# Optimization experiments

Hardware: AMD Instinct MI355X
Metric: run time of the kernel (lower is better)

Reference implementation:

```python
import jax, jax.numpy as jnp
import numpy as np

INPUT_SIZE = 512
HIDDEN_SIZE = 1024
BATCH = 32
SEQ = 512


def setup_inputs() -> dict:
    key = jax.random.key(0)
    ks = jax.random.split(key, 13)
    std = 1.0 / np.sqrt(HIDDEN_SIZE)
    u = lambda k, shape: jax.random.uniform(k, shape, jnp.float32, -std, std)
    X = jax.random.normal(ks[0], (BATCH, SEQ, INPUT_SIZE), jnp.float32)
    return {
        "X": X,
        "w_i": u(ks[1], (INPUT_SIZE, HIDDEN_SIZE)), "u_i": u(ks[2], (HIDDEN_SIZE, HIDDEN_SIZE)), "b_i": u(ks[3], (HIDDEN_SIZE,)),
        "w_f": u(ks[4], (INPUT_SIZE, HIDDEN_SIZE)), "u_f": u(ks[5], (HIDDEN_SIZE, HIDDEN_SIZE)), "b_f": u(ks[6], (HIDDEN_SIZE,)),
        "w_c": u(ks[7], (INPUT_SIZE, HIDDEN_SIZE)), "u_c": u(ks[8], (HIDDEN_SIZE, HIDDEN_SIZE)), "b_c": u(ks[9], (HIDDEN_SIZE,)),
        "w_o": u(ks[10], (INPUT_SIZE, HIDDEN_SIZE)), "u_o": u(ks[11], (HIDDEN_SIZE, HIDDEN_SIZE)), "b_o": u(ks[12], (HIDDEN_SIZE,)),
    }


def reference(X, w_i, u_i, b_i, w_f, u_f, b_f, w_c, u_c, b_c, w_o, u_o, b_o):
    bs, seq, _ = X.shape
    H = u_i.shape[0]
    # Precompute input-side projections for all gates in one batched matmul.
    W = jnp.concatenate([w_i, w_f, w_c, w_o], axis=1)        # [I, 4H]
    b = jnp.concatenate([b_i, b_f, b_c, b_o], axis=0)        # [4H]
    Xg = jnp.einsum("bsi,ig->bsg", X, W) + b                 # [B, S, 4H]
    Xg = jnp.transpose(Xg, (1, 0, 2))                         # [S, B, 4H]
    U = jnp.concatenate([u_i, u_f, u_c, u_o], axis=1)         # [H, 4H]

    def step(carry, xg_t):
        h, c = carry
        g = xg_t + h @ U                                       # [B, 4H]
        i_t = jax.nn.sigmoid(g[:, 0:H])
        f_t = jax.nn.sigmoid(g[:, H:2 * H])
        g_t = jnp.tanh(g[:, 2 * H:3 * H])
        o_t = jax.nn.sigmoid(g[:, 3 * H:4 * H])
        c_new = f_t * c + i_t * g_t
        h_new = o_t * jnp.tanh(c_new)
        return (h_new, c_new), h_new

    h0 = jnp.zeros((bs, H), X.dtype)
    c0 = jnp.zeros((bs, H), X.dtype)
    (h_t, c_t), hidden_seq = jax.lax.scan(step, (h0, c0), Xg)  # hidden_seq: [S, B, H]
    hidden_seq = jnp.transpose(hidden_seq, (1, 0, 2))          # [B, S, H]
    return hidden_seq, (h_t, c_t)
```

## Files before the change

kernel.cpp:

```cpp
#include <hip/hip_runtime.h>

typedef unsigned short u16;
typedef unsigned int   u32;

typedef __bf16 bf16x8 __attribute__((ext_vector_type(8)));
typedef float  f32x4  __attribute__((ext_vector_type(4)));
typedef u32    u32x4  __attribute__((ext_vector_type(4)));

#define B_ 32
#define S_ 512
#define I_ 512
#define H_ 1024
#define NB 64
#define UB 16
#define CB 64

#define XBF_U16   (S_ * B_ * I_)
#define HSLOT_B   65536

__device__ __forceinline__ u16 bf16bits(float f) {
    __bf16 b = (__bf16)f;
    return __builtin_bit_cast(u16, b);
}
__device__ __forceinline__ float sigmoid_(float x) { return 1.0f / (1.0f + __expf(-x)); }
__device__ __forceinline__ float tanh_(float x)    { return 2.0f / (1.0f + __expf(-2.0f * x)) - 1.0f; }

__global__ void __launch_bounds__(256)
xcvt(const float* __restrict__ X, u16* __restrict__ xbf)
{
    const int t = blockIdx.x, tid = threadIdx.x;
    #pragma unroll 4
    for (int b = 0; b < B_; ++b) {
        float2 v = *(const float2*)(X + (size_t)b * (S_ * I_) + (size_t)t * I_ + tid * 2);
        u32 pk = (u32)bf16bits(v.x) | ((u32)bf16bits(v.y) << 16);
        *(u32*)(xbf + (size_t)t * (B_ * I_) + b * I_ + tid * 2) = pk;
    }
}

__global__ void __launch_bounds__(512, 2)
lstm_rec(const u16* __restrict__ xbf,
         const float* __restrict__ u_i, const float* __restrict__ b_i,
         const float* __restrict__ u_f, const float* __restrict__ b_f,
         const float* __restrict__ u_c, const float* __restrict__ b_c,
         const float* __restrict__ u_o, const float* __restrict__ b_o,
         const float* __restrict__ w_i, const float* __restrict__ w_f,
         const float* __restrict__ w_c, const float* __restrict__ w_o,
         float* __restrict__ out, u16* __restrict__ hsl, u32* __restrict__ flags)
{
    __shared__ __align__(16) char  hx[32 * 3072];
    __shared__ __align__(16) float gb[4][32][68];

    const int tid  = threadIdx.x;
    const int bid  = blockIdx.x;
    const int wave = tid >> 6;
    const int lane = tid & 63;
    const int quad = lane >> 4;
    const int l16  = lane & 15;
    const int cg   = wave & 1;
    const int kq   = wave >> 1;

    bf16x8 bfr[2][12];
    #pragma unroll
    for (int cs = 0; cs < 2; ++cs) {
        const int gc = bid * CB + cg * 32 + cs * 16 + l16;
        const int ug = gc >> 2, g = gc & 3;
        const float* Up = ((g == 0) ? u_i : (g == 1) ? u_f : (g == 2) ? u_c : u_o) + ug;
        const float* Wp = ((g == 0) ? w_i : (g == 1) ? w_f : (g == 2) ? w_c : w_o) + ug;
        #pragma unroll
        for (int kb = 0; kb < 12; ++kb) {
            const int kbg = kq * 12 + kb;
            #pragma unroll
            for (int j = 0; j < 8; ++j) {
                const int k = kbg * 32 + quad * 8 + j;
                bfr[cs][kb][j] = (k < 1024) ? (__bf16)Up[(size_t)k * H_]
                                            : (__bf16)Wp[(size_t)(k - 1024) * H_];
            }
        }
    }

    const int srow = tid & 31;
    const int sch  = tid >> 5;
    const int skey = (srow & 7) << 4;
    char* sdst = hx + srow * 3072;
    const int akey = (l16 & 7) << 4;

    const int ub2  = tid >> 4;
    const int uq   = tid & 15;
    const int unit = bid * UB + uq;
    const float bia = b_i[unit], bif = b_f[unit], bic = b_c[unit], bio = b_o[unit];
    float cst = 0.0f;

    for (int t = 0; t < S_; ++t) {
        const u32x4* xsrc = (const u32x4*)(xbf + (size_t)t * (B_ * I_) + srow * I_ + sch * 32);
        u32x4 xv0 = xsrc[0], xv1 = xsrc[1], xv2 = xsrc[2], xv3 = xsrc[3];

        if (t) {
            if (wave == 0) {
                const u32* fp = flags + lane * 16;
                u32 v;
                do {
                    asm volatile("global_load_dword %0, %1, off sc0 sc1\n\t"
                                 "s_waitcnt vmcnt(0)"
                                 : "=v"(v) : "v"(fp) : "memory");
                } while ((int)v < t);
            }
            asm volatile("s_barrier" ::: "memory");

            const char* hsrc = (const char*)hsl + (size_t)(t & 1) * HSLOT_B
                               + srow * 2048 + sch * 128;
            u32x4 h0, h1, h2, h3, h4, h5, h6, h7;
            asm volatile(
                "global_load_dwordx4 %0, %8, off sc0 sc1\n\t"
                "global_load_dwordx4 %1, %8, off offset:16 sc0 sc1\n\t"
                "global_load_dwordx4 %2, %8, off offset:32 sc0 sc1\n\t"
                "global_load_dwordx4 %3, %8, off offset:48 sc0 sc1\n\t"
                "global_load_dwordx4 %4, %8, off offset:64 sc0 sc1\n\t"
                "global_load_dwordx4 %5, %8, off offset:80 sc0 sc1\n\t"
                "global_load_dwordx4 %6, %8, off offset:96 sc0 sc1\n\t"
                "global_load_dwordx4 %7, %8, off offset:112 sc0 sc1\n\t"
                "s_waitcnt vmcnt(0)"
                : "=&v"(h0), "=&v"(h1), "=&v"(h2), "=&v"(h3),
                  "=&v"(h4), "=&v"(h5), "=&v"(h6), "=&v"(h7)
                : "v"(hsrc) : "memory");
            *(u32x4*)(sdst + ((sch * 128 +   0) ^ skey)) = h0;
            *(u32x4*)(sdst + ((sch * 128 +  16) ^ skey)) = h1;
            *(u32x4*)(sdst + ((sch * 128 +  32) ^ skey)) = h2;
            *(u32x4*)(sdst + ((sch * 128 +  48) ^ skey)) = h3;
            *(u32x4*)(sdst + ((sch * 128 +  64) ^ skey)) = h4;
            *(u32x4*)(sdst + ((sch * 128 +  80) ^ skey)) = h5;
            *(u32x4*)(sdst + ((sch * 128 +  96) ^ skey)) = h6;
            *(u32x4*)(sdst + ((sch * 128 + 112) ^ skey)) = h7;
        } else {
            u32x4 z = {0u, 0u, 0u, 0u};
            #pragma unroll
            for (int i = 0; i < 8; ++i)
                *(u32x4*)(sdst + ((sch * 128 + i * 16) ^ skey)) = z;
        }
        *(u32x4*)(sdst + ((2048 + sch * 64 +  0) ^ skey)) = xv0;
        *(u32x4*)(sdst + ((2048 + sch * 64 + 16) ^ skey)) = xv1;
        *(u32x4*)(sdst + ((2048 + sch * 64 + 32) ^ skey)) = xv2;
        *(u32x4*)(sdst + ((2048 + sch * 64 + 48) ^ skey)) = xv3;
        __syncthreads();

        f32x4 a00 = {0.f, 0.f, 0.f, 0.f}, a01 = {0.f, 0.f, 0.f, 0.f};
        f32x4 a10 = {0.f, 0.f, 0.f, 0.f}, a11 = {0.f, 0.f, 0.f, 0.f};
        #pragma unroll
        for (int kb = 0; kb < 12; ++kb) {
            const int off = (kq * 12 + kb) * 64 + quad * 16;
            bf16x8 A0 = *(const bf16x8*)(hx + l16 * 3072 + (off ^ akey));
            bf16x8 A1 = *(const bf16x8*)(hx + (16 + l16) * 3072 + (off ^ akey));
            a00 = __builtin_amdgcn_mfma_f32_16x16x32_bf16(A0, bfr[0][kb], a00, 0, 0, 0);
            a10 = __builtin_amdgcn_mfma_f32_16x16x32_bf16(A1, bfr[0][kb], a10, 0, 0, 0);
            a01 = __builtin_amdgcn_mfma_f32_16x16x32_bf16(A0, bfr[1][kb], a01, 0, 0, 0);
            a11 = __builtin_amdgcn_mfma_f32_16x16x32_bf16(A1, bfr[1][kb], a11, 0, 0, 0);
        }
        #pragma unroll
        for (int r = 0; r < 4; ++r) {
            gb[kq][quad * 4 + r][cg * 32 + l16]           = a00[r];
            gb[kq][quad * 4 + r][cg * 32 + 16 + l16]      = a01[r];
            gb[kq][16 + quad * 4 + r][cg * 32 + l16]      = a10[r];
            gb[kq][16 + quad * 4 + r][cg * 32 + 16 + l16] = a11[r];
        }
        __syncthreads();

        f32x4 s0 = *(const f32x4*)&gb[0][ub2][uq * 4];
        f32x4 s1 = *(const f32x4*)&gb[1][ub2][uq * 4];
        f32x4 s2 = *(const f32x4*)&gb[2][ub2][uq * 4];
        f32x4 s3 = *(const f32x4*)&gb[3][ub2][uq * 4];
        f32x4 sg = s0 + s1 + s2 + s3;
        const float gi = sg[0] + bia, gf = sg[1] + bif;
        const float gc2 = sg[2] + bic, go = sg[3] + bio;
        cst = sigmoid_(gf) * cst + sigmoid_(gi) * tanh_(gc2);
        const float h = sigmoid_(go) * tanh_(cst);
        const float hn = __shfl_xor(h, 1);

        if ((tid & 1) == 0) {
            u32 pk = (u32)bf16bits(h) | ((u32)bf16bits(hn) << 16);
            char* hp = (char*)hsl + (size_t)((t + 1) & 1) * HSLOT_B + ub2 * 2048 + unit * 2;
            asm volatile("global_store_dword %0, %1, off sc0 sc1"
                         :: "v"(hp), "v"(pk) : "memory");
        }
        asm volatile("s_waitcnt vmcnt(0)" ::: "memory");
        asm volatile("s_barrier" ::: "memory");
        if (tid == 0) {
            u32* fp = flags + bid * 16;
            u32 fv = (u32)(t + 1);
            asm volatile("global_store_dword %0, %1, off sc0 sc1"
                         :: "v"(fp), "v"(fv) : "memory");
        }

        if ((tid & 1) == 0) {
            float2 o2; o2.x = h; o2.y = hn;
            *(float2*)(out + (size_t)ub2 * (S_ * H_) + (size_t)t * H_ + unit) = o2;
        }
        if (t == S_ - 1) {
            const float cn = __shfl_xor(cst, 1);
            if ((tid & 1) == 0) {
                float2 hf; hf.x = h;   hf.y = hn;
                float2 cf; cf.x = cst; cf.y = cn;
                *(float2*)(out + (size_t)B_ * S_ * H_ + ub2 * H_ + unit) = hf;
                *(float2*)(out + (size_t)B_ * S_ * H_ + B_ * H_ + ub2 * H_ + unit) = cf;
            }
        }
    }
}

extern "C" void kernel_launch(void* const* d_in, const int* in_sizes, int n_in,
                              void* d_out, int out_size, void* d_ws, size_t ws_size,
                              hipStream_t stream) {
    const float* X   = (const float*)d_in[0];
    const float* w_i = (const float*)d_in[1];
    const float* u_i = (const float*)d_in[2];
    const float* b_i = (const float*)d_in[3];
    const float* w_f = (const float*)d_in[4];
    const float* u_f = (const float*)d_in[5];
    const float* b_f = (const float*)d_in[6];
    const float* w_c = (const float*)d_in[7];
    const float* u_c = (const float*)d_in[8];
    const float* b_c = (const float*)d_in[9];
    const float* w_o = (const float*)d_in[10];
    const float* u_o = (const float*)d_in[11];
    const float* b_o = (const float*)d_in[12];
    float* out = (float*)d_out;

    u16* xbf   = (u16*)d_ws;
    u16* hsl   = (u16*)((char*)d_ws + (size_t)XBF_U16 * 2);
    u32* flags = (u32*)((char*)d_ws + (size_t)XBF_U16 * 2 + 2 * HSLOT_B);

    hipLaunchKernelGGL(xcvt, dim3(S_), dim3(256), 0, stream, X, xbf);
    hipLaunchKernelGGL(lstm_rec, dim3(NB), dim3(512), 0, stream,
                       xbf, u_i, b_i, u_f, b_f, u_c, b_c, u_o, b_o,
                       w_i, w_f, w_c, w_o, out, hsl, flags);
}
```

Baseline: 2.992 ms.

## Replace flag-based step sync with poisoned per-timestep hidden-state ring buffer

Result: slower. 4.282 ms (+43.1%).

```diff
diff --git a/kernel.cpp b/kernel.cpp
--- a/kernel.cpp
+++ b/kernel.cpp
@@ -15,8 +15,10 @@
 #define UB 16
 #define CB 64
 
-#define XBF_U16   (S_ * B_ * I_)
-#define HSLOT_B   65536
+#define XBF_U16  (S_ * B_ * I_)
+#define HSLOT_B  65536
+#define RING_N   (S_ + 1)
+#define POISON   0x7FC07FC0u
 
 __device__ __forceinline__ u16 bf16bits(float f) {
     __bf16 b = (__bf16)f;
@@ -24,6 +26,10 @@
 }
 __device__ __forceinline__ float sigmoid_(float x) { return 1.0f / (1.0f + __expf(-x)); }
 __device__ __forceinline__ float tanh_(float x)    { return 2.0f / (1.0f + __expf(-2.0f * x)) - 1.0f; }
+__device__ __forceinline__ u32 anyp(u32x4 v) {
+    return (u32)(v[0] == POISON) | (u32)(v[1] == POISON) |
+           (u32)(v[2] == POISON) | (u32)(v[3] == POISON);
+}
 
 __global__ void __launch_bounds__(256)
 xcvt(const float* __restrict__ X, u16* __restrict__ xbf)
@@ -34,6 +40,184 @@
         float2 v = *(const float2*)(X + (size_t)b * (S_ * I_) + (size_t)t * I_ + tid * 2);
         u32 pk = (u32)bf16bits(v.x) | ((u32)bf16bits(v.y) << 16);
         *(u32*)(xbf + (size_t)t * (B_ * I_) + b * I_ + tid * 2) = pk;
+    }
+}
+
+__global__ void __launch_bounds__(512, 2)
+lstm_ring(const u16* __restrict__ xbf,
+          const float* __restrict__ u_i, const float* __restrict__ b_i,
+          const float* __restrict__ u_f, const float* __restrict__ b_f,
+          const float* __restrict__ u_c, const float* __restrict__ b_c,
+          const float* __restrict__ u_o, const float* __restrict__ b_o,
+          const float* __restrict__ w_i, const float* __restrict__ w_f,
+          const float* __restrict__ w_c, const float* __restrict__ w_o,
+          float* __restrict__ out, u16* __restrict__ ring, u32* __restrict__ rdy)
+{
+    __shared__ __align__(16) char  hx[32 * 3072];
+    __shared__ __align__(16) float gb[4][32][68];
+
+    const int tid  = threadIdx.x;
+    const int bid  = blockIdx.x;
+    const int wave = tid >> 6;
+    const int lane = tid & 63;
+    const int quad = lane >> 4;
+    const int l16  = lane & 15;
+    const int cg   = wave & 1;
+    const int kq   = wave >> 1;
+
+    {
+        u32x4 pz; pz[0] = pz[1] = pz[2] = pz[3] = POISON;
+        #pragma unroll 4
+        for (int i = 0; i < 64; ++i) {
+            const int gidx = tid + i * 512;
+            const int s    = 1 + (gidx >> 6);
+            const int idx  = gidx & 63;
+            const int row  = idx >> 1, half = idx & 1;
+            char* pp = (char*)ring + (size_t)s * HSLOT_B + row * 2048 + bid * 32 + half * 16;
+            asm volatile("global_store_dwordx4 %0, %1, off sc0 sc1"
+                         :: "v"(pp), "v"(pz) : "memory");
+        }
+    }
+
+    bf16x8 bfr[2][12];
+    #pragma unroll
+    for (int cs = 0; cs < 2; ++cs) {
+        const int gc = bid * CB + cg * 32 + cs * 16 + l16;
+        const int ug = gc >> 2, g = gc & 3;
+        const float* Up = ((g == 0) ? u_i : (g == 1) ? u_f : (g == 2) ? u_c : u_o) + ug;
+        const float* Wp = ((g == 0) ? w_i : (g == 1) ? w_f : (g == 2) ? w_c : w_o) + ug;
+        #pragma unroll
+        for (int kb = 0; kb < 12; ++kb) {
+            const int kbg = kq * 12 + kb;
+            #pragma unroll
+            for (int j = 0; j < 8; ++j) {
+                const int k = kbg * 32 + quad * 8 + j;
+                bfr[cs][kb][j] = (k < 1024) ? (__bf16)Up[(size_t)k * H_]
+                                            : (__bf16)Wp[(size_t)(k - 1024) * H_];
+            }
+        }
+    }
+
+    asm volatile("s_waitcnt vmcnt(0)" ::: "memory");
+    if (tid == 0) {
+        u32* rp = rdy + bid * 16; u32 one = 1u;
+        asm volatile("global_store_dword %0, %1, off sc0 sc1" :: "v"(rp), "v"(one) : "memory");
+    }
+    if (wave == 0) {
+        const u32* rp = rdy + lane * 16;
+        u32 v;
+        do {
+            asm volatile("global_load_dword %0, %1, off sc0 sc1\n\ts_waitcnt vmcnt(0)"
+                         : "=v"(v) : "v"(rp) : "memory");
+        } while ((int)v < 1);
+    }
+    asm volatile("s_barrier" ::: "memory");
+
+    const int srow = tid & 31;
+    const int sch  = tid >> 5;
+    const int skey = (srow & 7) << 4;
+    char* sdst = hx + srow * 3072;
+    const int akey = (l16 & 7) << 4;
+
+    const int ub2  = tid >> 4;
+    const int uq   = tid & 15;
+    const int unit = bid * UB + uq;
+    const float bia = b_i[unit], bif = b_f[unit], bic = b_c[unit], bio = b_o[unit];
+    float cst = 0.0f;
+
+    for (int t = 0; t < S_; ++t) {
+        const u32x4* xsrc = (const u32x4*)(xbf + (size_t)t * (B_ * I_) + srow * I_ + sch * 32);
+        u32x4 xv0 = xsrc[0], xv1 = xsrc[1], xv2 = xsrc[2], xv3 = xsrc[3];
+
+        if (t) {
+            const char* hsrc = (const char*)ring + (size_t)t * HSLOT_B + srow * 2048 + sch * 128;
+            u32x4 h0, h1, h2, h3, h4, h5, h6, h7;
+            for (;;) {
+                asm volatile(
+                    "global_load_dwordx4 %0, %8, off sc0 sc1\n\t"
+                    "global_load_dwordx4 %1, %8, off offset:16 sc0 sc1\n\t"
+                    "global_load_dwordx4 %2, %8, off offset:32 sc0 sc1\n\t"
+                    "global_load_dwordx4 %3, %8, off offset:48 sc0 sc1\n\t"
+                    "global_load_dwordx4 %4, %8, off offset:64 sc0 sc1\n\t"
+                    "global_load_dwordx4 %5, %8, off offset:80 sc0 sc1\n\t"
+                    "global_load_dwordx4 %6, %8, off offset:96 sc0 sc1\n\t"
+                    "global_load_dwordx4 %7, %8, off offset:112 sc0 sc1\n\t"
+                    "s_waitcnt vmcnt(0)"
+                    : "=&v"(h0), "=&v"(h1), "=&v"(h2), "=&v"(h3),
+                      "=&v"(h4), "=&v"(h5), "=&v"(h6), "=&v"(h7)
+                    : "v"(hsrc) : "memory");
+                if (!(anyp(h0) | anyp(h1) | anyp(h2) | anyp(h3) |
+                      anyp(h4) | anyp(h5) | anyp(h6) | anyp(h7))) break;
+            }
+            *(u32x4*)(sdst + ((sch * 128 +   0) ^ skey)) = h0;
+            *(u32x4*)(sdst + ((sch * 128 +  16) ^ skey)) = h1;
+            *(u32x4*)(sdst + ((sch * 128 +  32) ^ skey)) = h2;
+            *(u32x4*)(sdst + ((sch * 128 +  48) ^ skey)) = h3;
+            *(u32x4*)(sdst + ((sch * 128 +  64) ^ skey)) = h4;
+            *(u32x4*)(sdst + ((sch * 128 +  80) ^ skey)) = h5;
+            *(u32x4*)(sdst + ((sch * 128 +  96) ^ skey)) = h6;
+            *(u32x4*)(sdst + ((sch * 128 + 112) ^ skey)) = h7;
+        } else {
+            u32x4 z = {0u, 0u, 0u, 0u};
+            #pragma unroll
+            for (int i = 0; i < 8; ++i)
+                *(u32x4*)(sdst + ((sch * 128 + i * 16) ^ skey)) = z;
+        }
+        *(u32x4*)(sdst + ((2048 + sch * 64 +  0) ^ skey)) = xv0;
+        *(u32x4*)(sdst + ((2048 + sch * 64 + 16) ^ skey)) = xv1;
+        *(u32x4*)(sdst + ((2048 + sch * 64 + 32) ^ skey)) = xv2;
+        *(u32x4*)(sdst + ((2048 + sch * 64 + 48) ^ skey)) = xv3;
+        __syncthreads();
+
+        f32x4 a00 = {0.f, 0.f, 0.f, 0.f}, a01 = {0.f, 0.f, 0.f, 0.f};
+        f32x4 a10 = {0.f, 0.f, 0.f, 0.f}, a11 = {0.f, 0.f, 0.f, 0.f};
+        #pragma unroll
+        for (int kb = 0; kb < 12; ++kb) {
+            const int off = (kq * 12 + kb) * 64 + quad * 16;
+            bf16x8 A0 = *(const bf16x8*)(hx + l16 * 3072 + (off ^ akey));
+            bf16x8 A1 = *(const bf16x8*)(hx + (16 + l16) * 3072 + (off ^ akey));
+            a00 = __builtin_amdgcn_mfma_f32_16x16x32_bf16(A0, bfr[0][kb], a00, 0, 0, 0);
+            a10 = __builtin_amdgcn_mfma_f32_16x16x32_bf16(A1, bfr[0][kb], a10, 0, 0, 0);
+            a01 = __builtin_amdgcn_mfma_f32_16x16x32_bf16(A0, bfr[1][kb], a01, 0, 0, 0);
+            a11 = __builtin_amdgcn_mfma_f32_16x16x32_bf16(A1, bfr[1][kb], a11, 0, 0, 0);
+        }
+        #pragma unroll
+        for (int r = 0; r < 4; ++r) {
+            gb[kq][quad * 4 + r][cg * 32 + l16]           = a00[r];
+            gb[kq][quad * 4 + r][cg * 32 + 16 + l16]      = a01[r];
+            gb[kq][16 + quad * 4 + r][cg * 32 + l16]      = a10[r];
+            gb[kq][16 + quad * 4 + r][cg * 32 + 16 + l16] = a11[r];
+        }
+        __syncthreads();
+
+        f32x4 s0 = *(const f32x4*)&gb[0][ub2][uq * 4];
+        f32x4 s1 = *(const f32x4*)&gb[1][ub2][uq * 4];
+        f32x4 s2 = *(const f32x4*)&gb[2][ub2][uq * 4];
+        f32x4 s3 = *(const f32x4*)&gb[3][ub2][uq * 4];
+        f32x4 sg = s0 + s1 + s2 + s3;
+        const float gi = sg[0] + bia, gf = sg[1] + bif;
+        const float gc2 = sg[2] + bic, go = sg[3] + bio;
+        cst = sigmoid_(gf) * cst + sigmoid_(gi) * tanh_(gc2);
+        const float h = sigmoid_(go) * tanh_(cst);
+        const float hn = __shfl_xor(h, 1);
+
+        if ((tid & 1) == 0) {
+            u32 pk = (u32)bf16bits(h) | ((u32)bf16bits(hn) << 16);
+            char* hp = (char*)ring + (size_t)(t + 1) * HSLOT_B + ub2 * 2048 + unit * 2;
+            asm volatile("global_store_dword %0, %1, off sc0 sc1"
+                         :: "v"(hp), "v"(pk) : "memory");
+            float2 o2; o2.x = h; o2.y = hn;
+            *(float2*)(out + (size_t)ub2 * (S_ * H_) + (size_t)t * H_ + unit) = o2;
+        }
+        if (t == S_ - 1) {
+            const float cn = __shfl_xor(cst, 1);
+            if ((tid & 1) == 0) {
+                float2 hf; hf.x = h;   hf.y = hn;
+                float2 cf; cf.x = cst; cf.y = cn;
+                *(float2*)(out + (size_t)B_ * S_ * H_ + ub2 * H_ + unit) = hf;
+                *(float2*)(out + (size_t)B_ * S_ * H_ + B_ * H_ + ub2 * H_ + unit) = cf;
+            }
+        }
     }
 }
 
@@ -223,12 +407,23 @@
     const float* b_o = (const float*)d_in[12];
     float* out = (float*)d_out;
 
-    u16* xbf   = (u16*)d_ws;
-    u16* hsl   = (u16*)((char*)d_ws + (size_t)XBF_U16 * 2);
-    u32* flags = (u32*)((char*)d_ws + (size_t)XBF_U16 * 2 + 2 * HSLOT_B);
+    const size_t xbf_b  = (size_t)XBF_U16 * 2;
+    const size_t ring_b = (size_t)RING_N * HSLOT_B;
+    u16* xbf = (u16*)d_ws;
 
     hipLaunchKernelGGL(xcvt, dim3(S_), dim3(256), 0, stream, X, xbf);
-    hipLaunchKernelGGL(lstm_rec, dim3(NB), dim3(512), 0, stream,
-                       xbf, u_i, b_i, u_f, b_f, u_c, b_c, u_o, b_o,
-                       w_i, w_f, w_c, w_o, out, hsl, flags);
-}
+
+    if (ws_size >= xbf_b + ring_b + 8192) {
+        u16* ring = (u16*)((char*)d_ws + xbf_b);
+        u32* rdy  = (u32*)((char*)d_ws + xbf_b + ring_b);
+        hipLaunchKernelGGL(lstm_ring, dim3(NB), dim3(512), 0, stream,
+                           xbf, u_i, b_i, u_f, b_f, u_c, b_c, u_o, b_o,
+                           w_i, w_f, w_c, w_o, out, ring, rdy);
+    } else {
+        u16* hsl   = (u16*)((char*)d_ws + xbf_b);
+        u32* flags = (u32*)((char*)d_ws + xbf_b + 2 * HSLOT_B);
+        hipLaunchKernelGGL(lstm_rec, dim3(NB), dim3(512), 0, stream,
+                           xbf, u_i, b_i, u_f, b_f, u_c, b_c, u_o, b_o,
+                           w_i, w_f, w_c, w_o, out, hsl, flags);
+    }
+}
```
